# Optimization experiments

Hardware: AMD Instinct MI355X
Metric: run time of the kernel (lower is better)

Reference implementation:

```python
import jax, jax.numpy as jnp
import numpy as np

BETA = 0.25
NUM_EMBEDDINGS = 512
DIM_EMBEDDING = 64


def setup_inputs() -> dict:
    key = jax.random.key(0)
    k1, k2 = jax.random.split(key)
    z_e = jax.random.normal(k1, (32, 64, 64, 64), dtype=jnp.float32)
    # torch init: uniform_(-1/num_embeddings, 1/num_embeddings)
    lim = 1.0 / NUM_EMBEDDINGS
    embeddings = jax.random.uniform(
        k2, (NUM_EMBEDDINGS, DIM_EMBEDDING), dtype=jnp.float32,
        minval=-lim, maxval=lim)
    return {"z_e": z_e, "embeddings": embeddings}


def reference(z_e, embeddings):
    # Flatten exactly as torch's z_e.view(-1, dim_embedding) on (N,C,H,W)
    z_flat = z_e.reshape(-1, DIM_EMBEDDING)          # [M, D]
    # Squared euclidean distances: ||z||^2 + ||e||^2 - 2 z e^T
    distances = (
        jnp.sum(z_flat ** 2, axis=1, keepdims=True)
        + jnp.sum(embeddings ** 2, axis=1)
        - 2.0 * jnp.matmul(z_flat, embeddings.T)
    )                                                # [M, K]
    encoding_indices = jnp.argmin(distances, axis=1)[:, None]  # [M, 1]
    quantized = embeddings[encoding_indices[:, 0]].reshape(z_e.shape)
    # Straight-through estimator
    quantized_st = z_e + jax.lax.stop_gradient(quantized - z_e)
    recon_loss = jnp.mean((jax.lax.stop_gradient(quantized_st) - z_e) ** 2)
    commitment_loss = BETA * jnp.mean(
        (quantized_st - jax.lax.stop_gradient(z_e)) ** 2)
    loss = recon_loss + commitment_loss
    return (loss, quantized_st, encoding_indices)
```

## Files before the change

kernel.cpp:

```cpp
#include <hip/hip_runtime.h>
#include <hip/hip_bf16.h>

constexpr int NELEM = 8388608;
constexpr int ROWS  = 64;
constexpr int NBLK  = 131072 / ROWS;
constexpr int ZS    = 68;
constexpr float EPS = 1e-3f;
constexpr int QCAP  = 1024;

typedef short bf16x8 __attribute__((ext_vector_type(8)));
typedef float v4f    __attribute__((ext_vector_type(4)));

__device__ bf16x8 g_efrag[32][2][64];
__device__ float  g_en2[512];

__device__ inline bf16x8 cvt_hi8(const float* __restrict__ s, float scale) {
    bf16x8 h;
#pragma unroll
    for (int j = 0; j < 8; ++j) {
        __hip_bfloat16 b = __float2bfloat16(scale * s[j]);
        h[j] = (short)__bfloat16_as_ushort(b);
    }
    return h;
}

__global__ void __launch_bounds__(256) vq_prep(const float* __restrict__ emb,
                                               float* __restrict__ out) {
    const int b = blockIdx.x;
    if (b < 16) {
        const int id   = b * 256 + threadIdx.x;
        const int lane = id & 63;
        const int kc   = (id >> 6) & 1;
        const int ct   = id >> 7;
        const float* src = emb + (size_t)(ct * 16 + (lane & 15)) * 64
                               + kc * 32 + (lane >> 4) * 8;
        g_efrag[ct][kc][lane] = cvt_hi8(src, -2.0f);
    } else {
#pragma unroll
        for (int c = 0; c < 2; ++c) {
            const int k = threadIdx.x + c * 256;
            const float4* e4 = (const float4*)(emb + (size_t)k * 64);
            float a = 0.f, bq = 0.f, cc = 0.f, d = 0.f;
#pragma unroll
            for (int i = 0; i < 16; ++i) {
                float4 v = e4[i];
                a += v.x * v.x; bq += v.y * v.y; cc += v.z * v.z; d += v.w * v.w;
            }
            g_en2[k] = (a + bq) + (cc + d);
        }
        if (threadIdx.x == 0) out[0] = 0.f;
    }
}

__global__ __launch_bounds__(256) __attribute__((amdgpu_waves_per_eu(2, 2)))
void vq_main(const float* __restrict__ z,
             const float* __restrict__ emb,
             float* __restrict__ out) {
    __shared__ float s_z[ROWS * ZS];
    __shared__ float s_en2[512];
    __shared__ float s_zn2[ROWS];
    __shared__ unsigned long long s_key[ROWS];
    __shared__ float s_wmin[ROWS][4];
    __shared__ float s_thr[ROWS];
    __shared__ unsigned s_q[QCAP];
    __shared__ int s_qn;
    __shared__ float s_lpart[4];

    const int tid  = threadIdx.x;
    const int lane = tid & 63;
    const int wid  = __builtin_amdgcn_readfirstlane(tid >> 6);
    const int mcol = lane & 15;
    const int quad = lane >> 4;

    {
        const int row = tid >> 2, seg = tid & 3;
        const float4* gp = (const float4*)(z + ((size_t)blockIdx.x * ROWS + row) * 64 + seg * 16);
#pragma unroll
        for (int i = 0; i < 4; ++i)
            *(float4*)&s_z[row * ZS + seg * 16 + i * 4] = gp[i];
    }
    s_en2[tid]       = g_en2[tid];
    s_en2[tid + 256] = g_en2[tid + 256];
    if (tid < ROWS) s_key[tid] = ~0ULL;
    if (tid == 0) s_qn = 0;
    __syncthreads();

    if (tid < ROWS) {
        const float* zr = &s_z[tid * ZS];
        float a = 0.f, b = 0.f, c = 0.f, d = 0.f;
#pragma unroll
        for (int i = 0; i < 16; ++i) {
            a += zr[4*i]   * zr[4*i];   b += zr[4*i+1] * zr[4*i+1];
            c += zr[4*i+2] * zr[4*i+2]; d += zr[4*i+3] * zr[4*i+3];
        }
        s_zn2[tid] = (a + b) + (c + d);
    }

    bf16x8 zf[4][2];
#pragma unroll
    for (int rg = 0; rg < 4; ++rg) {
        zf[rg][0] = cvt_hi8(&s_z[(rg * 16 + mcol) * ZS +  0 + quad * 8], 1.0f);
        zf[rg][1] = cvt_hi8(&s_z[(rg * 16 + mcol) * ZS + 32 + quad * 8], 1.0f);
    }

    v4f acc[4][8];
    float lmin[4];
#pragma unroll
    for (int rg = 0; rg < 4; ++rg) lmin[rg] = 3.402823466e38f;
#pragma unroll
    for (int ct = 0; ct < 8; ++ct) {
        const int gct = wid * 8 + ct;
        bf16x8 e0 = g_efrag[gct][0][lane];
        bf16x8 e1 = g_efrag[gct][1][lane];
        v4f base = *(const v4f*)&s_en2[gct * 16 + quad * 4];
#pragma unroll
        for (int rg = 0; rg < 4; ++rg) {
            v4f a = base;
            a = __builtin_amdgcn_mfma_f32_16x16x32_bf16(e0, zf[rg][0], a, 0, 0, 0);
            a = __builtin_amdgcn_mfma_f32_16x16x32_bf16(e1, zf[rg][1], a, 0, 0, 0);
            acc[rg][ct] = a;
            lmin[rg] = fminf(lmin[rg], fminf(fminf(a.x, a.y), fminf(a.z, a.w)));
        }
    }

#pragma unroll
    for (int rg = 0; rg < 4; ++rg) {
        float m = lmin[rg];
        m = fminf(m, __shfl_xor(m, 16, 64));
        m = fminf(m, __shfl_xor(m, 32, 64));
        if (quad == 0) s_wmin[rg * 16 + mcol][wid] = m;
    }
    __syncthreads();
    if (tid < ROWS)
        s_thr[tid] = fminf(fminf(s_wmin[tid][0], s_wmin[tid][1]),
                           fminf(s_wmin[tid][2], s_wmin[tid][3])) + EPS;
    __syncthreads();

#pragma unroll
    for (int rg = 0; rg < 4; ++rg) {
        const int row = rg * 16 + mcol;
        const float thr = s_thr[row];
#pragma unroll
        for (int ct = 0; ct < 8; ++ct) {
            v4f a = acc[rg][ct];
            float m4 = fminf(fminf(a.x, a.y), fminf(a.z, a.w));
            if (m4 <= thr) {
#pragma unroll
                for (int r = 0; r < 4; ++r) {
                    if (a[r] <= thr) {
                        int slot = atomicAdd(&s_qn, 1);
                        if (slot < QCAP)
                            s_q[slot] = ((unsigned)row << 16) |
                                        (unsigned)(wid * 128 + ct * 16 + quad * 4 + r);
                    }
                }
            }
        }
    }
    __syncthreads();

    {
        const int qn = s_qn;
        for (int i = tid; i < qn && i < QCAP; i += 256) {
            const unsigned e = s_q[i];
            const int row = e >> 16, code = e & 0xFFFF;
            const float* zr = &s_z[row * ZS];
            const float* er = emb + (size_t)code * 64;
            float a = 0.f, b = 0.f, c2 = 0.f, d = 0.f;
#pragma unroll
            for (int g = 0; g < 16; ++g) {
                a  += zr[4*g]   * er[4*g];   b += zr[4*g+1] * er[4*g+1];
                c2 += zr[4*g+2] * er[4*g+2]; d += zr[4*g+3] * er[4*g+3];
            }
            float dot  = (a + b) + (c2 + d);
            float dist = (s_zn2[row] + s_en2[code]) - 2.0f * dot;
            unsigned long long key =
                ((unsigned long long)__float_as_uint(dist) << 32) | (unsigned)code;
            atomicMin(&s_key[row], key);
        }
    }
    __syncthreads();

    const int row = tid >> 2, seg = tid & 3;
    const int widx = (int)(unsigned)(s_key[row] & 0x1FFULL);
    const float* er = emb + (size_t)widx * 64 + seg * 16;
    const float* zr = &s_z[row * ZS + seg * 16];
    float* qo = out + 1 + ((size_t)blockIdx.x * ROWS + row) * 64 + seg * 16;
    float lsum = 0.f;
#pragma unroll
    for (int j = 0; j < 16; ++j) {
        float zv = zr[j], ev = er[j];
        float q = zv + (ev - zv);
        float df = q - zv; lsum += df * df;
        qo[j] = q;
    }
    if (seg == 0)
        out[1 + NELEM + blockIdx.x * ROWS + row] = (float)widx;

#pragma unroll
    for (int off = 32; off; off >>= 1) lsum += __shfl_down(lsum, off, 64);
    if (lane == 0) s_lpart[wid] = lsum;
    __syncthreads();
    if (tid == 0) {
        float p = (s_lpart[0] + s_lpart[1]) + (s_lpart[2] + s_lpart[3]);
        atomicAdd(out, p * (1.25f / 8388608.0f));
    }
}

extern "C" void kernel_launch(void* const* d_in, const int* in_sizes, int n_in,
                              void* d_out, int out_size, void* d_ws, size_t ws_size,
                              hipStream_t stream) {
    const float* z   = (const float*)d_in[0];
    const float* emb = (const float*)d_in[1];
    float* out = (float*)d_out;

    vq_prep<<<17, 256, 0, stream>>>(emb, out);
    vq_main<<<NBLK, 256, 0, stream>>>(z, emb, out);
}
```

Before: 134.7 us.

## Recompute MFMA distances instead of holding accumulators to raise occupancy

Drops the 128-register accumulator array and recomputes the bf16 MFMA distance tiles in a second pass for candidate collection. This cuts register pressure so the waves-per-EU hint can rise from 2 to 4, giving more latency hiding for the memory-bound loads. The row-norm computation is also spread over all 256 threads with shuffles instead of 64. The cost is doubling the MFMA work and re-reading the embedding fragments.

```diff
diff --git a/kernel.cpp b/kernel.cpp
--- a/kernel.cpp
+++ b/kernel.cpp
@@ -52,7 +52,7 @@
     }
 }
 
-__global__ __launch_bounds__(256) __attribute__((amdgpu_waves_per_eu(2, 2)))
+__global__ __launch_bounds__(256) __attribute__((amdgpu_waves_per_eu(4)))
 void vq_main(const float* __restrict__ z,
              const float* __restrict__ emb,
              float* __restrict__ out) {
@@ -85,15 +85,15 @@
     if (tid == 0) s_qn = 0;
     __syncthreads();
 
-    if (tid < ROWS) {
-        const float* zr = &s_z[tid * ZS];
-        float a = 0.f, b = 0.f, c = 0.f, d = 0.f;
-#pragma unroll
-        for (int i = 0; i < 16; ++i) {
-            a += zr[4*i]   * zr[4*i];   b += zr[4*i+1] * zr[4*i+1];
-            c += zr[4*i+2] * zr[4*i+2]; d += zr[4*i+3] * zr[4*i+3];
-        }
-        s_zn2[tid] = (a + b) + (c + d);
+    {
+        const int row = tid >> 2, s = tid & 3;
+        const float* zr = &s_z[row * ZS];
+        float p = 0.f;
+#pragma unroll
+        for (int i = 0; i < 16; ++i) p += zr[4 * i + s] * zr[4 * i + s];
+        p += __shfl_xor(p, 1, 64);
+        p += __shfl_xor(p, 2, 64);
+        if (s == 0) s_zn2[row] = p;
     }
 
     bf16x8 zf[4][2];
@@ -103,7 +103,6 @@
         zf[rg][1] = cvt_hi8(&s_z[(rg * 16 + mcol) * ZS + 32 + quad * 8], 1.0f);
     }
 
-    v4f acc[4][8];
     float lmin[4];
 #pragma unroll
     for (int rg = 0; rg < 4; ++rg) lmin[rg] = 3.402823466e38f;
@@ -118,7 +117,6 @@
             v4f a = base;
             a = __builtin_amdgcn_mfma_f32_16x16x32_bf16(e0, zf[rg][0], a, 0, 0, 0);
             a = __builtin_amdgcn_mfma_f32_16x16x32_bf16(e1, zf[rg][1], a, 0, 0, 0);
-            acc[rg][ct] = a;
             lmin[rg] = fminf(lmin[rg], fminf(fminf(a.x, a.y), fminf(a.z, a.w)));
         }
     }
@@ -136,21 +134,28 @@
                            fminf(s_wmin[tid][2], s_wmin[tid][3])) + EPS;
     __syncthreads();
 
-#pragma unroll
-    for (int rg = 0; rg < 4; ++rg) {
-        const int row = rg * 16 + mcol;
-        const float thr = s_thr[row];
-#pragma unroll
-        for (int ct = 0; ct < 8; ++ct) {
-            v4f a = acc[rg][ct];
+    float thr[4];
+#pragma unroll
+    for (int rg = 0; rg < 4; ++rg) thr[rg] = s_thr[rg * 16 + mcol];
+#pragma unroll
+    for (int ct = 0; ct < 8; ++ct) {
+        const int gct = wid * 8 + ct;
+        bf16x8 e0 = g_efrag[gct][0][lane];
+        bf16x8 e1 = g_efrag[gct][1][lane];
+        v4f base = *(const v4f*)&s_en2[gct * 16 + quad * 4];
+#pragma unroll
+        for (int rg = 0; rg < 4; ++rg) {
+            v4f a = base;
+            a = __builtin_amdgcn_mfma_f32_16x16x32_bf16(e0, zf[rg][0], a, 0, 0, 0);
+            a = __builtin_amdgcn_mfma_f32_16x16x32_bf16(e1, zf[rg][1], a, 0, 0, 0);
             float m4 = fminf(fminf(a.x, a.y), fminf(a.z, a.w));
-            if (m4 <= thr) {
+            if (m4 <= thr[rg]) {
 #pragma unroll
                 for (int r = 0; r < 4; ++r) {
-                    if (a[r] <= thr) {
+                    if (a[r] <= thr[rg]) {
                         int slot = atomicAdd(&s_qn, 1);
                         if (slot < QCAP)
-                            s_q[slot] = ((unsigned)row << 16) |
+                            s_q[slot] = ((unsigned)(rg * 16 + mcol) << 16) |
                                         (unsigned)(wid * 128 + ct * 16 + quad * 4 + r);
                     }
                 }
```

Result: slower. 159.5 us (+18.4%).
